# Kernel tuning notes

Hardware: AMD Instinct MI355X
Metric: run time of the kernel (lower is better)

The kernel has to match this reference:

```python
import jax, jax.numpy as jnp
import numpy as np

N = 100000
E = 1600000
D = 128

def _degrees(idx, n):
    d = jax.ops.segment_sum(jnp.ones(idx.shape[0], jnp.float32), idx, num_segments=n)
    return jnp.clip(d, 1.0)

def _gconv(feat, src, dst, W, b, residual, act):
    n = feat.shape[0]
    norm_out = _degrees(src, n) ** -0.5            # [N] out-degree norm
    h = feat * norm_out[:, None]                   # scale src features
    msgs = h[src]                                  # gather [E, D]
    agg = jax.ops.segment_sum(msgs, dst, num_segments=n)  # scatter-sum [N, D]
    rst = agg @ W.T + b                            # dense linear
    norm_in = _degrees(dst, n) ** -0.5             # [N] in-degree norm
    rst = rst * norm_in[:, None]
    if residual:
        rst = rst + feat                           # identity residual (in==out)
    if act:
        rst = jax.nn.relu(rst)
    return rst

def setup_inputs() -> dict:
    key = jax.random.key(0)
    ks = jax.random.split(key, 10)
    feat = jax.random.normal(ks[0], (N, D), jnp.float32)
    src = jax.random.randint(ks[1], (E,), 0, N)
    dst = jax.random.randint(ks[2], (E,), 0, N)
    s = 1.0 / np.sqrt(D)
    W1 = jax.random.uniform(ks[3], (D, D), jnp.float32, -s, s)
    b1 = jax.random.uniform(ks[4], (D,), jnp.float32, -s, s)
    W2 = jax.random.uniform(ks[5], (D, D), jnp.float32, -s, s)
    b2 = jax.random.uniform(ks[6], (D,), jnp.float32, -s, s)
    W3 = jax.random.uniform(ks[7], (D, D), jnp.float32, -s, s)
    b3 = jax.random.uniform(ks[8], (D,), jnp.float32, -s, s)
    return {"feat": feat, "src": src, "dst": dst,
            "W1": W1, "b1": b1, "W2": W2, "b2": b2, "W3": W3, "b3": b3}

def reference(feat, src, dst, W1, b1, W2, b2, W3, b3):
    # 3-layer GCN, dropout=0, norm=None, encoding=False:
    # layers 0,1: residual + relu; layer 2: no residual, no activation
    h = _gconv(feat, src, dst, W1, b1, residual=True, act=True)
    h = _gconv(h, src, dst, W2, b2, residual=True, act=True)
    h = _gconv(h, src, dst, W3, b3, residual=False, act=False)
    return h
```

## Files before the change

kernel.cpp:

```cpp
#include <hip/hip_runtime.h>

#define NN 100000
#define EE 1600000
#define DD 128
#define NB 512
#define CAP 4608
#define CHUNK 8192

typedef __attribute__((ext_vector_type(8))) short short8v;
typedef __attribute__((ext_vector_type(4))) float f32x4;
typedef __attribute__((ext_vector_type(8))) unsigned short ushort8v;

#define LROW 136

static __device__ __forceinline__ unsigned short f2bf(float x) {
  unsigned u = __builtin_bit_cast(unsigned, x);
  return (unsigned short)((u + 0x7FFFu + ((u >> 16) & 1u)) >> 16);
}
static __device__ __forceinline__ float bf2f(unsigned short u) {
  return __builtin_bit_cast(float, (unsigned)u << 16);
}

__global__ __launch_bounds__(512) void initcur_k(int* __restrict__ cur_d,
                                                 int* __restrict__ cur_s) {
  int t = threadIdx.x;
  cur_d[t] = t * CAP;
  cur_s[t] = t * CAP;
}

__global__ __launch_bounds__(256) void split_k(const int* __restrict__ src,
                                               const int* __restrict__ dst,
                                               int* __restrict__ cur_d,
                                               int* __restrict__ cur_s,
                                               unsigned* __restrict__ tmp_d,
                                               unsigned char* __restrict__ tmp_s) {
  __shared__ int hd[NB], hs[NB], bd[NB], bs[NB];
  int t = threadIdx.x;
  int base = blockIdx.x * CHUNK;
  int end = base + CHUNK < EE ? base + CHUNK : EE;
  for (int b = t; b < NB; b += 256) { hd[b] = 0; hs[b] = 0; }
  __syncthreads();
  for (int i = base + t; i < end; i += 256) {
    atomicAdd(&hd[dst[i] >> 8], 1);
    atomicAdd(&hs[src[i] >> 8], 1);
  }
  __syncthreads();
  for (int b = t; b < NB; b += 256) {
    bd[b] = hd[b] ? atomicAdd(&cur_d[b], hd[b]) : 0;
    bs[b] = hs[b] ? atomicAdd(&cur_s[b], hs[b]) : 0;
    hd[b] = 0;
    hs[b] = 0;
  }
  __syncthreads();
  for (int i = base + t; i < end; i += 256) {
    int s = src[i];
    int d = dst[i];
    int bin = d >> 8;
    int r = atomicAdd(&hd[bin], 1);
    int pos = bd[bin] + r;
    if (pos < (bin + 1) * CAP) tmp_d[pos] = ((unsigned)(d & 255) << 17) | (unsigned)s;
    bin = s >> 8;
    r = atomicAdd(&hs[bin], 1);
    pos = bs[bin] + r;
    if (pos < (bin + 1) * CAP) tmp_s[pos] = (unsigned char)(s & 255);
  }
}

__global__ __launch_bounds__(512) void scan512_k(const int* __restrict__ cur_d,
                                                 int* __restrict__ dstart) {
  __shared__ int lds[512];
  int t = threadIdx.x;
  int v = cur_d[t] - t * CAP;
  v = v < CAP ? v : CAP;
  lds[t] = v;
  __syncthreads();
  int run = v;
  for (int off = 1; off < 512; off <<= 1) {
    int y = (t >= off) ? lds[t - off] : 0;
    __syncthreads();
    run += y;
    lds[t] = run;
    __syncthreads();
  }
  dstart[t] = run - v;
}

__global__ __launch_bounds__(256) void bucket_dst_k(const unsigned* __restrict__ tmp_d,
                                                    const int* __restrict__ cur_d,
                                                    const int* __restrict__ dstart,
                                                    int* __restrict__ csr,
                                                    int* __restrict__ row_s,
                                                    int* __restrict__ row_e,
                                                    float* __restrict__ norm_in) {
  __shared__ unsigned stage[CAP];
  __shared__ int h[256], sc[256], rk[256];
  int b = blockIdx.x;
  int t = threadIdx.x;
  int cnt = cur_d[b] - b * CAP;
  cnt = cnt < CAP ? cnt : CAP;
  int ds = dstart[b];
  for (int i = t; i < cnt; i += 256) stage[i] = tmp_d[b * CAP + i];
  h[t] = 0;
  __syncthreads();
  for (int i = t; i < cnt; i += 256) atomicAdd(&h[stage[i] >> 17], 1);
  __syncthreads();
  int v = h[t];
  sc[t] = v;
  __syncthreads();
  int run = v;
  for (int off = 1; off < 256; off <<= 1) {
    int y = (t >= off) ? sc[t - off] : 0;
    __syncthreads();
    run += y;
    sc[t] = run;
    __syncthreads();
  }
  int excl = run - v;
  int n = b * 256 + t;
  if (n < NN) {
    row_s[n] = ds + excl;
    row_e[n] = ds + excl + v;
    norm_in[n] = rsqrtf((float)(v > 1 ? v : 1));
  }
  rk[t] = excl;
  __syncthreads();
  for (int i = t; i < cnt; i += 256) {
    unsigned w = stage[i];
    int r = atomicAdd(&rk[w >> 17], 1);
    csr[ds + r] = (int)(w & 0x1FFFFu);
  }
}

__global__ __launch_bounds__(256) void bucket_src_k(const unsigned char* __restrict__ tmp_s,
                                                    const int* __restrict__ cur_s,
                                                    float* __restrict__ norm_out) {
  __shared__ int h[256];
  int b = blockIdx.x;
  int t = threadIdx.x;
  int cnt = cur_s[b] - b * CAP;
  cnt = cnt < CAP ? cnt : CAP;
  h[t] = 0;
  __syncthreads();
  const unsigned char* p = tmp_s + b * CAP;
  for (int i = t; i < cnt; i += 256) atomicAdd(&h[p[i]], 1);
  __syncthreads();
  int n = b * 256 + t;
  if (n < NN) norm_out[n] = rsqrtf((float)(h[t] > 1 ? h[t] : 1));
}

__global__ __launch_bounds__(256) void wconv_k(const float* __restrict__ w,
                                               unsigned short* __restrict__ o) {
  int i = blockIdx.x * 256 + threadIdx.x;
  float4 v = *reinterpret_cast<const float4*>(w + i * 4);
  ushort4 pk = make_ushort4(f2bf(v.x), f2bf(v.y), f2bf(v.z), f2bf(v.w));
  *reinterpret_cast<ushort4*>(o + i * 4) = pk;
}

__global__ __launch_bounds__(256) void hconv_k(const float* __restrict__ feat,
                                               const float* __restrict__ no,
                                               unsigned short* __restrict__ h) {
  int i = blockIdx.x * 256 + threadIdx.x;
  int node = i >> 4;
  int lane = i & 15;
  float n = no[node];
  const float* p = feat + node * DD + lane * 8;
  float4 a = *reinterpret_cast<const float4*>(p);
  float4 b = *reinterpret_cast<const float4*>(p + 4);
  ushort8v o;
  o[0] = f2bf(a.x * n); o[1] = f2bf(a.y * n); o[2] = f2bf(a.z * n); o[3] = f2bf(a.w * n);
  o[4] = f2bf(b.x * n); o[5] = f2bf(b.y * n); o[6] = f2bf(b.z * n); o[7] = f2bf(b.w * n);
  *reinterpret_cast<ushort8v*>(h + node * DD + lane * 8) = o;
}

__global__ __launch_bounds__(256) void layer_k(const unsigned short* __restrict__ h,
                                               const int* __restrict__ csr,
                                               const int* __restrict__ row_s,
                                               const int* __restrict__ row_e,
                                               const unsigned short* __restrict__ Wb,
                                               const float* __restrict__ bias,
                                               const float* __restrict__ nin,
                                               const float* __restrict__ nout,
                                               const float* __restrict__ resid,
                                               float* __restrict__ outp,
                                               unsigned short* __restrict__ hnext,
                                               int mode) {
  __shared__ unsigned short tile[16 * LROW];
  int t = threadIdx.x;
  int n16 = t >> 4;
  int c = t & 15;
  int node = blockIdx.x * 16 + n16;

  int e0 = row_s[node];
  int e1 = row_e[node];
  float acc[8] = {0.f, 0.f, 0.f, 0.f, 0.f, 0.f, 0.f, 0.f};
  int e = e0;
  for (; e + 2 <= e1; e += 2) {
    int s0 = csr[e];
    int s1 = csr[e + 1];
    ushort8v u = *reinterpret_cast<const ushort8v*>(h + (size_t)s0 * DD + c * 8);
    ushort8v v = *reinterpret_cast<const ushort8v*>(h + (size_t)s1 * DD + c * 8);
#pragma unroll
    for (int i = 0; i < 8; ++i) acc[i] += bf2f(u[i]) + bf2f(v[i]);
  }
  if (e < e1) {
    int s0 = csr[e];
    ushort8v u = *reinterpret_cast<const ushort8v*>(h + (size_t)s0 * DD + c * 8);
#pragma unroll
    for (int i = 0; i < 8; ++i) acc[i] += bf2f(u[i]);
  }
  ushort8v o;
#pragma unroll
  for (int i = 0; i < 8; ++i) o[i] = f2bf(acc[i]);
  *reinterpret_cast<ushort8v*>(&tile[n16 * LROW + c * 8]) = o;
  __syncthreads();

  int wid = t >> 6;
  int lane = t & 63;
  int l15 = lane & 15;
  int kgrp = lane >> 4;
  int mynode = blockIdx.x * 16 + l15;

  const unsigned short* bp = &tile[l15 * LROW + kgrp * 8];
  short8v b0 = *reinterpret_cast<const short8v*>(bp);
  short8v b1 = *reinterpret_cast<const short8v*>(bp + 32);
  short8v b2 = *reinterpret_cast<const short8v*>(bp + 64);
  short8v b3 = *reinterpret_cast<const short8v*>(bp + 96);

  int epnode = blockIdx.x * 16 + l15;
  float ninv = nin[epnode];
  float noutv = (mode != 0) ? nout[epnode] : 0.f;

#pragma unroll
  for (int q = 0; q < 2; ++q) {
    int ct = wid * 2 + q;
    const unsigned short* wp = Wb + (size_t)(ct * 16 + l15) * DD + kgrp * 8;
    short8v w0 = *reinterpret_cast<const short8v*>(wp);
    short8v w1 = *reinterpret_cast<const short8v*>(wp + 32);
    short8v w2 = *reinterpret_cast<const short8v*>(wp + 64);
    short8v w3 = *reinterpret_cast<const short8v*>(wp + 96);
    f32x4 cacc = {0.f, 0.f, 0.f, 0.f};
    cacc = __builtin_amdgcn_mfma_f32_16x16x32_bf16(w0, b0, cacc, 0, 0, 0);
    cacc = __builtin_amdgcn_mfma_f32_16x16x32_bf16(w1, b1, cacc, 0, 0, 0);
    cacc = __builtin_amdgcn_mfma_f32_16x16x32_bf16(w2, b2, cacc, 0, 0, 0);
    cacc = __builtin_amdgcn_mfma_f32_16x16x32_bf16(w3, b3, cacc, 0, 0, 0);

    int j = ct * 16 + kgrp * 4;
    float4 bj = *reinterpret_cast<const float4*>(bias + j);
    size_t idx = (size_t)epnode * DD + j;
    float4 v;
    v.x = (cacc[0] + bj.x) * ninv;
    v.y = (cacc[1] + bj.y) * ninv;
    v.z = (cacc[2] + bj.z) * ninv;
    v.w = (cacc[3] + bj.w) * ninv;
    if (mode != 0) {
      float4 rs = *reinterpret_cast<const float4*>(resid + idx);
      v.x = fmaxf(v.x + rs.x, 0.f);
      v.y = fmaxf(v.y + rs.y, 0.f);
      v.z = fmaxf(v.z + rs.z, 0.f);
      v.w = fmaxf(v.w + rs.w, 0.f);
      if (mode == 1) *reinterpret_cast<float4*>(outp + idx) = v;
      ushort4 hn = make_ushort4(f2bf(v.x * noutv), f2bf(v.y * noutv),
                                f2bf(v.z * noutv), f2bf(v.w * noutv));
      *reinterpret_cast<ushort4*>(hnext + idx) = hn;
    } else {
      *reinterpret_cast<float4*>(outp + idx) = v;
    }
  }
}

extern "C" void kernel_launch(void* const* d_in, const int* in_sizes, int n_in,
                              void* d_out, int out_size, void* d_ws, size_t ws_size,
                              hipStream_t stream) {
  const float* feat = (const float*)d_in[0];
  const int* src = (const int*)d_in[1];
  const int* dst = (const int*)d_in[2];
  const float* W1 = (const float*)d_in[3];
  const float* b1 = (const float*)d_in[4];
  const float* W2 = (const float*)d_in[5];
  const float* b2 = (const float*)d_in[6];
  const float* W3 = (const float*)d_in[7];
  const float* b3 = (const float*)d_in[8];
  float* out = (float*)d_out;

  int* row_s = (int*)d_ws;
  int* row_e = row_s + NN;
  float* norm_out = (float*)(row_e + NN);
  float* norm_in = norm_out + NN;
  int* cur_d = (int*)(norm_in + NN);
  int* cur_s = cur_d + NB;
  int* dstart = cur_s + NB;
  int* pad = dstart + NB;
  unsigned short* Wbf = (unsigned short*)pad;
  int* csr = (int*)(Wbf + 3 * 16384);
  unsigned short* hbuf = (unsigned short*)(csr + EE);
  unsigned short* hbuf2 = hbuf + (size_t)NN * DD;

  unsigned* tmp_d = (unsigned*)d_out;
  unsigned char* tmp_s = (unsigned char*)d_out + (size_t)NB * CAP * 4;

  initcur_k<<<1, 512, 0, stream>>>(cur_d, cur_s);
  split_k<<<(EE + CHUNK - 1) / CHUNK, 256, 0, stream>>>(src, dst, cur_d, cur_s, tmp_d, tmp_s);
  scan512_k<<<1, 512, 0, stream>>>(cur_d, dstart);
  bucket_dst_k<<<NB, 256, 0, stream>>>(tmp_d, cur_d, dstart, csr, row_s, row_e, norm_in);
  bucket_src_k<<<NB, 256, 0, stream>>>(tmp_s, cur_s, norm_out);

  wconv_k<<<16, 256, 0, stream>>>(W1, Wbf);
  wconv_k<<<16, 256, 0, stream>>>(W2, Wbf + 16384);
  wconv_k<<<16, 256, 0, stream>>>(W3, Wbf + 32768);
  hconv_k<<<6250, 256, 0, stream>>>(feat, norm_out, hbuf);

  layer_k<<<6250, 256, 0, stream>>>(hbuf, csr, row_s, row_e, Wbf, b1, norm_in,
                                    norm_out, feat, out, hbuf2, 1);
  layer_k<<<6250, 256, 0, stream>>>(hbuf2, csr, row_s, row_e, Wbf + 16384, b2, norm_in,
                                    norm_out, out, nullptr, hbuf, 2);
  layer_k<<<6250, 256, 0, stream>>>(hbuf, csr, row_s, row_e, Wbf + 32768, b3, norm_in,
                                    norm_out, nullptr, out, nullptr, 0);
}
```

Before: 357.1 us.

## Keep intermediate activations in bf16 and apply source norm during gather

Intermediate layer outputs are now stored only as unscaled bf16, and the out-degree normalisation is applied per edge inside the gather loop rather than baked into the stored features. This removes the fp32 intermediate write in layer one and halves the residual read in layer two, and the feature-prep kernel becomes a plain bf16 cast. In exchange, each edge costs an extra scalar load of the source norm plus a multiply. The residual is also now carried in bf16, which lowers precision.

```diff
diff --git a/kernel.cpp b/kernel.cpp
--- a/kernel.cpp
+++ b/kernel.cpp
@@ -148,7 +148,7 @@
   if (n < NN) norm_out[n] = rsqrtf((float)(h[t] > 1 ? h[t] : 1));
 }
 
-__global__ __launch_bounds__(256) void wconv_k(const float* __restrict__ w,
+__global__ __launch_bounds__(256) void bconv_k(const float* __restrict__ w,
                                                unsigned short* __restrict__ o) {
   int i = blockIdx.x * 256 + threadIdx.x;
   float4 v = *reinterpret_cast<const float4*>(w + i * 4);
@@ -156,33 +156,18 @@
   *reinterpret_cast<ushort4*>(o + i * 4) = pk;
 }
 
-__global__ __launch_bounds__(256) void hconv_k(const float* __restrict__ feat,
-                                               const float* __restrict__ no,
-                                               unsigned short* __restrict__ h) {
-  int i = blockIdx.x * 256 + threadIdx.x;
-  int node = i >> 4;
-  int lane = i & 15;
-  float n = no[node];
-  const float* p = feat + node * DD + lane * 8;
-  float4 a = *reinterpret_cast<const float4*>(p);
-  float4 b = *reinterpret_cast<const float4*>(p + 4);
-  ushort8v o;
-  o[0] = f2bf(a.x * n); o[1] = f2bf(a.y * n); o[2] = f2bf(a.z * n); o[3] = f2bf(a.w * n);
-  o[4] = f2bf(b.x * n); o[5] = f2bf(b.y * n); o[6] = f2bf(b.z * n); o[7] = f2bf(b.w * n);
-  *reinterpret_cast<ushort8v*>(h + node * DD + lane * 8) = o;
-}
-
 __global__ __launch_bounds__(256) void layer_k(const unsigned short* __restrict__ h,
                                                const int* __restrict__ csr,
                                                const int* __restrict__ row_s,
                                                const int* __restrict__ row_e,
+                                               const float* __restrict__ nsrc,
                                                const unsigned short* __restrict__ Wb,
                                                const float* __restrict__ bias,
                                                const float* __restrict__ nin,
-                                               const float* __restrict__ nout,
-                                               const float* __restrict__ resid,
-                                               float* __restrict__ outp,
-                                               unsigned short* __restrict__ hnext,
+                                               const float* __restrict__ residf,
+                                               const unsigned short* __restrict__ residb,
+                                               float* __restrict__ outf,
+                                               unsigned short* __restrict__ outb,
                                                int mode) {
   __shared__ unsigned short tile[16 * LROW];
   int t = threadIdx.x;
@@ -197,16 +182,19 @@
   for (; e + 2 <= e1; e += 2) {
     int s0 = csr[e];
     int s1 = csr[e + 1];
+    float n0 = nsrc[s0];
+    float n1 = nsrc[s1];
     ushort8v u = *reinterpret_cast<const ushort8v*>(h + (size_t)s0 * DD + c * 8);
     ushort8v v = *reinterpret_cast<const ushort8v*>(h + (size_t)s1 * DD + c * 8);
 #pragma unroll
-    for (int i = 0; i < 8; ++i) acc[i] += bf2f(u[i]) + bf2f(v[i]);
+    for (int i = 0; i < 8; ++i) acc[i] += bf2f(u[i]) * n0 + bf2f(v[i]) * n1;
   }
   if (e < e1) {
     int s0 = csr[e];
+    float n0 = nsrc[s0];
     ushort8v u = *reinterpret_cast<const ushort8v*>(h + (size_t)s0 * DD + c * 8);
 #pragma unroll
-    for (int i = 0; i < 8; ++i) acc[i] += bf2f(u[i]);
+    for (int i = 0; i < 8; ++i) acc[i] += bf2f(u[i]) * n0;
   }
   ushort8v o;
 #pragma unroll
@@ -218,7 +206,6 @@
   int lane = t & 63;
   int l15 = lane & 15;
   int kgrp = lane >> 4;
-  int mynode = blockIdx.x * 16 + l15;
 
   const unsigned short* bp = &tile[l15 * LROW + kgrp * 8];
   short8v b0 = *reinterpret_cast<const short8v*>(bp);
@@ -228,7 +215,6 @@
 
   int epnode = blockIdx.x * 16 + l15;
   float ninv = nin[epnode];
-  float noutv = (mode != 0) ? nout[epnode] : 0.f;
 
 #pragma unroll
   for (int q = 0; q < 2; ++q) {
@@ -252,18 +238,24 @@
     v.y = (cacc[1] + bj.y) * ninv;
     v.z = (cacc[2] + bj.z) * ninv;
     v.w = (cacc[3] + bj.w) * ninv;
-    if (mode != 0) {
-      float4 rs = *reinterpret_cast<const float4*>(resid + idx);
+    if (mode == 1) {
+      float4 rs = *reinterpret_cast<const float4*>(residf + idx);
       v.x = fmaxf(v.x + rs.x, 0.f);
       v.y = fmaxf(v.y + rs.y, 0.f);
       v.z = fmaxf(v.z + rs.z, 0.f);
       v.w = fmaxf(v.w + rs.w, 0.f);
-      if (mode == 1) *reinterpret_cast<float4*>(outp + idx) = v;
-      ushort4 hn = make_ushort4(f2bf(v.x * noutv), f2bf(v.y * noutv),
-                                f2bf(v.z * noutv), f2bf(v.w * noutv));
-      *reinterpret_cast<ushort4*>(hnext + idx) = hn;
+      ushort4 hn = make_ushort4(f2bf(v.x), f2bf(v.y), f2bf(v.z), f2bf(v.w));
+      *reinterpret_cast<ushort4*>(outb + idx) = hn;
+    } else if (mode == 3) {
+      ushort4 rs = *reinterpret_cast<const ushort4*>(residb + idx);
+      v.x = fmaxf(v.x + bf2f(rs.x), 0.f);
+      v.y = fmaxf(v.y + bf2f(rs.y), 0.f);
+      v.z = fmaxf(v.z + bf2f(rs.z), 0.f);
+      v.w = fmaxf(v.w + bf2f(rs.w), 0.f);
+      ushort4 hn = make_ushort4(f2bf(v.x), f2bf(v.y), f2bf(v.z), f2bf(v.w));
+      *reinterpret_cast<ushort4*>(outb + idx) = hn;
     } else {
-      *reinterpret_cast<float4*>(outp + idx) = v;
+      *reinterpret_cast<float4*>(outf + idx) = v;
     }
   }
 }
@@ -292,8 +284,8 @@
   int* pad = dstart + NB;
   unsigned short* Wbf = (unsigned short*)pad;
   int* csr = (int*)(Wbf + 3 * 16384);
-  unsigned short* hbuf = (unsigned short*)(csr + EE);
-  unsigned short* hbuf2 = hbuf + (size_t)NN * DD;
+  unsigned short* vb1 = (unsigned short*)(csr + EE);
+  unsigned short* vb2 = vb1 + (size_t)NN * DD;
 
   unsigned* tmp_d = (unsigned*)d_out;
   unsigned char* tmp_s = (unsigned char*)d_out + (size_t)NB * CAP * 4;
@@ -304,15 +296,15 @@
   bucket_dst_k<<<NB, 256, 0, stream>>>(tmp_d, cur_d, dstart, csr, row_s, row_e, norm_in);
   bucket_src_k<<<NB, 256, 0, stream>>>(tmp_s, cur_s, norm_out);
 
-  wconv_k<<<16, 256, 0, stream>>>(W1, Wbf);
-  wconv_k<<<16, 256, 0, stream>>>(W2, Wbf + 16384);
-  wconv_k<<<16, 256, 0, stream>>>(W3, Wbf + 32768);
-  hconv_k<<<6250, 256, 0, stream>>>(feat, norm_out, hbuf);
-
-  layer_k<<<6250, 256, 0, stream>>>(hbuf, csr, row_s, row_e, Wbf, b1, norm_in,
-                                    norm_out, feat, out, hbuf2, 1);
-  layer_k<<<6250, 256, 0, stream>>>(hbuf2, csr, row_s, row_e, Wbf + 16384, b2, norm_in,
-                                    norm_out, out, nullptr, hbuf, 2);
-  layer_k<<<6250, 256, 0, stream>>>(hbuf, csr, row_s, row_e, Wbf + 32768, b3, norm_in,
-                                    norm_out, nullptr, out, nullptr, 0);
-}
+  bconv_k<<<16, 256, 0, stream>>>(W1, Wbf);
+  bconv_k<<<16, 256, 0, stream>>>(W2, Wbf + 16384);
+  bconv_k<<<16, 256, 0, stream>>>(W3, Wbf + 32768);
+  bconv_k<<<12500, 256, 0, stream>>>(feat, vb1);
+
+  layer_k<<<6250, 256, 0, stream>>>(vb1, csr, row_s, row_e, norm_out, Wbf, b1,
+                                    norm_in, feat, nullptr, nullptr, vb2, 1);
+  layer_k<<<6250, 256, 0, stream>>>(vb2, csr, row_s, row_e, norm_out, Wbf + 16384, b2,
+                                    norm_in, nullptr, vb2, nullptr, vb1, 3);
+  layer_k<<<6250, 256, 0, stream>>>(vb1, csr, row_s, row_e, norm_out, Wbf + 32768, b3,
+                                    norm_in, nullptr, nullptr, out, nullptr, 0);
+}
```

Measured after the change: 349.2 us. 1.02x faster.
